# Performance work log

Hardware: AMD Instinct MI355X
Metric: run time of the kernel (lower is better)

The kernel has to match this reference:

```python
import jax, jax.numpy as jnp
import numpy as np

MARGIN = 0.2


def setup_inputs() -> dict:
    key = jax.random.key(0)
    k1, k2 = jax.random.split(key)
    B, D, C = 4096, 512, 512
    embeddings = jax.random.normal(k1, (B, D), dtype=jnp.float32)
    labels = jax.random.randint(k2, (B,), 0, C, dtype=jnp.int64)
    return {"embeddings": embeddings, "labels": labels}


def reference(embeddings, labels):
    B = embeddings.shape[0]
    # L2-normalize rows (eps matches torch F.normalize default 1e-12)
    norm = jnp.maximum(jnp.linalg.norm(embeddings, axis=1, keepdims=True), 1e-12)
    e = embeddings / norm
    # cosine distance matrix [B, B]
    dist = 1.0 - e @ e.T
    same = labels[:, None] == labels[None, :]
    eye = jnp.eye(B, dtype=bool)
    pos_mask = same & ~eye
    neg_mask = ~same
    # dist in [0, 2]; sentinels outside that range for masked reductions
    hardest_pos = jnp.max(jnp.where(pos_mask, dist, -1.0), axis=1)
    hardest_neg = jnp.min(jnp.where(neg_mask, dist, 3.0), axis=1)
    valid = jnp.any(pos_mask, axis=1) & jnp.any(neg_mask, axis=1)
    per_anchor = jax.nn.relu(hardest_pos - hardest_neg + MARGIN)
    loss_sum = jnp.sum(jnp.where(valid, per_anchor, 0.0))
    n_valid = jnp.maximum(jnp.sum(valid.astype(jnp.int32)), 1)
    return loss_sum / n_valid.astype(embeddings.dtype)
```

## Files before the change

kernel.cpp:

```cpp
#include <hip/hip_runtime.h>
#include <hip/hip_bf16.h>

#define BDIM 4096
#define DDIM 512
#define BT 128
#define BK 32
#define NKT (DDIM / BK)
#define NPAN (BDIM / BT)
#define NTRI (NPAN * (NPAN + 1) / 2)

typedef __bf16 bf16x8 __attribute__((ext_vector_type(8)));
typedef float f32x4 __attribute__((ext_vector_type(4)));
typedef unsigned short ushort_t;

__device__ inline ushort_t f2bf(float f) {
  __hip_bfloat16 h = __float2bfloat16(f);
  return *reinterpret_cast<ushort_t*>(&h);
}

__device__ inline unsigned int enc_f32(float x) {
  unsigned int u = __float_as_uint(x);
  return (u & 0x80000000u) ? ~u : (u | 0x80000000u);
}
__device__ inline float dec_f32(unsigned int e) {
  unsigned int u = (e & 0x80000000u) ? (e ^ 0x80000000u) : ~e;
  return __uint_as_float(u);
}

__global__ __launch_bounds__(256) void norm_kernel(const float* __restrict__ x,
                                                   ushort_t* __restrict__ e,
                                                   unsigned int* __restrict__ minpos_e,
                                                   unsigned int* __restrict__ maxneg_e) {
  if (blockIdx.x == 0) {
    const unsigned int init_min = enc_f32(1e30f);
    const unsigned int init_max = enc_f32(-1e30f);
    for (int i = threadIdx.x; i < BDIM; i += 256) {
      minpos_e[i] = init_min;
      maxneg_e[i] = init_max;
    }
  }
  const int row  = blockIdx.x * 4 + (threadIdx.x >> 6);
  const int lane = threadIdx.x & 63;
  const float4* xr = reinterpret_cast<const float4*>(x + (size_t)row * DDIM);
  float4 v0 = xr[lane];
  float4 v1 = xr[lane + 64];
  float ss = v0.x*v0.x + v0.y*v0.y + v0.z*v0.z + v0.w*v0.w
           + v1.x*v1.x + v1.y*v1.y + v1.z*v1.z + v1.w*v1.w;
#pragma unroll
  for (int off = 32; off >= 1; off >>= 1) ss += __shfl_xor(ss, off);
  const float inv = 1.0f / fmaxf(sqrtf(ss), 1e-12f);

  ushort4 p0, p1;
  p0.x = f2bf(v0.x * inv); p0.y = f2bf(v0.y * inv);
  p0.z = f2bf(v0.z * inv); p0.w = f2bf(v0.w * inv);
  p1.x = f2bf(v1.x * inv); p1.y = f2bf(v1.y * inv);
  p1.z = f2bf(v1.z * inv); p1.w = f2bf(v1.w * inv);
  ushort4* er = reinterpret_cast<ushort4*>(e + (size_t)row * DDIM);
  er[lane]      = p0;
  er[lane + 64] = p1;
}

#define STAGE(buf, kt)                                                         \
  do {                                                                         \
    _Pragma("unroll")                                                          \
    for (int q = 0; q < 4; ++q) {                                              \
      if (q >= 2 && diag) continue;            \
      const int off  = q * 4096 + tid * 16;                      \
      const int loff = off & 8191;                                             \
      const int row  = loff >> 6;                                              \
      const int kb   = loff & 63;                                              \
      const int pan  = (q < 2) ? Ibase : Jbase;                                \
      const char* src = (const char*)e + (size_t)(pan + row) * (DDIM * 2) +    \
                        (kt) * 64 + kb;                                        \
      __builtin_amdgcn_global_load_lds(                                        \
          (const __attribute__((address_space(1))) void*)src,                  \
          (__attribute__((address_space(3))) void*)(&Blds[buf][off]),          \
          16, 0, 0);                                                           \
    }                                                                          \
  } while (0)

__global__ __launch_bounds__(256, 4) void gemm_reduce_kernel(
    const ushort_t* __restrict__ e, const int* __restrict__ labels,
    unsigned int* __restrict__ minpos_e, unsigned int* __restrict__ maxneg_e) {
  __shared__ __align__(16) char Blds[2][16384];
  __shared__ int Llab[256];

  const int tid  = threadIdx.x;
  const int wave = tid >> 6;
  const int lane = tid & 63;
  const int l15  = lane & 15;
  const int g    = lane >> 4;
  const int wr   = wave >> 1;
  const int wc   = wave & 1;

  const int bid = blockIdx.x;
  const int t   = (bid & 7) * (NTRI / 8) + (bid >> 3);
  int I = (int)((65.0f - sqrtf(4225.0f - 8.0f * (float)t)) * 0.5f);
  while (32 * (I + 1) - ((I + 1) * I) / 2 <= t) ++I;
  while (32 * I - (I * (I - 1)) / 2 > t) --I;
  const int J = I + (t - (32 * I - (I * (I - 1)) / 2));
  const int Ibase = I * BT;
  const int Jbase = J * BT;
  const bool diag = (I == J);

  if (tid < 128) Llab[tid] = labels[Ibase + tid];
  else           Llab[tid] = labels[Jbase + tid - 128];

  f32x4 acc[4][4];
#pragma unroll
  for (int m = 0; m < 4; ++m)
#pragma unroll
    for (int n = 0; n < 4; ++n) acc[m][n] = (f32x4){0.f, 0.f, 0.f, 0.f};

  STAGE(0, 0);
  __syncthreads();

  const int bofs = diag ? 0 : 8192;
  for (int kt = 0; kt < NKT; ++kt) {
    if (kt + 1 < NKT) STAGE((kt + 1) & 1, kt + 1);

    const char* Ab = Blds[kt & 1];
    const char* Bb = Blds[kt & 1] + bofs;
    bf16x8 a[4], b[4];
#pragma unroll
    for (int m = 0; m < 4; ++m)
      a[m] = *reinterpret_cast<const bf16x8*>(
          Ab + (wr * 64 + m * 16 + l15) * 64 + g * 16);
#pragma unroll
    for (int n = 0; n < 4; ++n)
      b[n] = *reinterpret_cast<const bf16x8*>(
          Bb + (wc * 64 + n * 16 + l15) * 64 + g * 16);
#pragma unroll
    for (int m = 0; m < 4; ++m)
#pragma unroll
      for (int n = 0; n < 4; ++n)
        acc[m][n] = __builtin_amdgcn_mfma_f32_16x16x32_bf16(a[m], b[n],
                                                            acc[m][n], 0, 0, 0);
    __syncthreads();
  }

  float cmp[4], cmx[4];
  int lj[4], gj[4];
#pragma unroll
  for (int n = 0; n < 4; ++n) {
    cmp[n] = 1e30f; cmx[n] = -1e30f;
    gj[n]  = Jbase + wc * 64 + n * 16 + l15;
    lj[n]  = Llab[128 + wc * 64 + n * 16 + l15];
  }
  float rmp[4][4], rmx[4][4];
#pragma unroll
  for (int m = 0; m < 4; ++m)
#pragma unroll
    for (int r = 0; r < 4; ++r) { rmp[m][r] = 1e30f; rmx[m][r] = -1e30f; }

#pragma unroll
  for (int m = 0; m < 4; ++m) {
#pragma unroll
    for (int r = 0; r < 4; ++r) {
      const int rloc = wr * 64 + m * 16 + g * 4 + r;
      const int li   = Llab[rloc];
      const int gi   = Ibase + rloc;
#pragma unroll
      for (int n = 0; n < 4; ++n) {
        const float v = acc[m][n][r];
        if (li == lj[n]) {
          if (gi != gj[n]) {
            rmp[m][r] = fminf(rmp[m][r], v);
            cmp[n]    = fminf(cmp[n], v);
          }
        } else {
          rmx[m][r] = fmaxf(rmx[m][r], v);
          cmx[n]    = fmaxf(cmx[n], v);
        }
      }
    }
  }

#pragma unroll
  for (int off = 16; off <= 32; off <<= 1) {
#pragma unroll
    for (int n = 0; n < 4; ++n) {
      cmp[n] = fminf(cmp[n], __shfl_xor(cmp[n], off));
      cmx[n] = fmaxf(cmx[n], __shfl_xor(cmx[n], off));
    }
  }
#pragma unroll
  for (int off = 1; off < 16; off <<= 1) {
#pragma unroll
    for (int m = 0; m < 4; ++m)
#pragma unroll
      for (int r = 0; r < 4; ++r) {
        rmp[m][r] = fminf(rmp[m][r], __shfl_xor(rmp[m][r], off));
        rmx[m][r] = fmaxf(rmx[m][r], __shfl_xor(rmx[m][r], off));
      }
  }

  if (g == 0) {
#pragma unroll
    for (int n = 0; n < 4; ++n) {
      if (cmp[n] < 1e29f)  atomicMin(&minpos_e[gj[n]], enc_f32(cmp[n]));
      if (cmx[n] > -1e29f) atomicMax(&maxneg_e[gj[n]], enc_f32(cmx[n]));
    }
  }
  if (l15 == 0) {
#pragma unroll
    for (int m = 0; m < 4; ++m)
#pragma unroll
      for (int r = 0; r < 4; ++r) {
        const int gi = Ibase + wr * 64 + m * 16 + g * 4 + r;
        if (rmp[m][r] < 1e29f)  atomicMin(&minpos_e[gi], enc_f32(rmp[m][r]));
        if (rmx[m][r] > -1e29f) atomicMax(&maxneg_e[gi], enc_f32(rmx[m][r]));
      }
  }
}

__global__ __launch_bounds__(1024) void finalize_kernel(
    const unsigned int* __restrict__ minpos_e, const unsigned int* __restrict__ maxneg_e,
    float* __restrict__ out) {
  const int tid = threadIdx.x;
  float sum = 0.f;
  int cnt = 0;
  for (int row = tid; row < BDIM; row += 1024) {
    const float mp = dec_f32(minpos_e[row]);
    const float mn = dec_f32(maxneg_e[row]);
    if (mp < 1e29f && mn > -1e29f) {
      sum += fmaxf(0.f, mn - mp + 0.2f);
      cnt += 1;
    }
  }
#pragma unroll
  for (int off = 32; off >= 1; off >>= 1) {
    sum += __shfl_xor(sum, off);
    cnt += __shfl_xor(cnt, off);
  }
  __shared__ float wsum[16];
  __shared__ int   wcnt[16];
  const int wv = tid >> 6, ln = tid & 63;
  if (ln == 0) { wsum[wv] = sum; wcnt[wv] = cnt; }
  __syncthreads();
  if (tid == 0) {
    float S = 0.f; int C = 0;
    for (int w = 0; w < 16; ++w) { S += wsum[w]; C += wcnt[w]; }
    out[0] = S / (float)(C > 0 ? C : 1);
  }
}

extern "C" void kernel_launch(void* const* d_in, const int* in_sizes, int n_in,
                              void* d_out, int out_size, void* d_ws, size_t ws_size,
                              hipStream_t stream) {
  const float* x      = (const float*)d_in[0];
  const int*   labels = (const int*)d_in[1];
  float* out = (float*)d_out;

  char* ws = (char*)d_ws;
  ushort_t* e            = (ushort_t*)ws;
  unsigned int* minpos_e = (unsigned int*)(ws + (size_t)BDIM * DDIM * 2);
  unsigned int* maxneg_e = minpos_e + BDIM;

  norm_kernel<<<BDIM / 4, 256, 0, stream>>>(x, e, minpos_e, maxneg_e);
  gemm_reduce_kernel<<<NTRI, 256, 0, stream>>>(e, labels, minpos_e, maxneg_e);
  finalize_kernel<<<1, 1024, 0, stream>>>(minpos_e, maxneg_e, out);
}
```

Before: 36.68 us.

## Use 128x64 triangle tiles, triple-buffered LDS pipeline, and fused last-block finalize

The triangular 128x128 tiling becomes 128x64 tiles over the upper triangle (1056 blocks), so diagonal blocks no longer need special handling and more blocks are available for load balancing. The K loop moves to a three-stage LDS ring with explicit vmcnt waits and raw barriers, and sets MFMA priority, to overlap global-to-LDS loads with compute. Labels are now read straight from global memory instead of being staged in LDS. The separate finalize kernel is replaced by a last-block-done atomic counter inside the GEMM kernel, which saves a launch but adds a threadfence and an atomic per block.

Result: slower. 106.3 us (+189.8%).

```diff
diff --git a/kernel.cpp b/kernel.cpp
--- a/kernel.cpp
+++ b/kernel.cpp
@@ -3,16 +3,20 @@
 
 #define BDIM 4096
 #define DDIM 512
-#define BT 128
+#define BTI 128
+#define BTJ 64
 #define BK 32
 #define NKT (DDIM / BK)
-#define NPAN (BDIM / BT)
-#define NTRI (NPAN * (NPAN + 1) / 2)
+#define NBLK 1056
 
 typedef __bf16 bf16x8 __attribute__((ext_vector_type(8)));
 typedef float f32x4 __attribute__((ext_vector_type(4)));
 typedef unsigned short ushort_t;
 
+#define WAITV3() asm volatile("s_waitcnt vmcnt(3)" ::: "memory")
+#define WAITV0() asm volatile("s_waitcnt vmcnt(0)" ::: "memory")
+#define WAITL0() asm volatile("s_waitcnt lgkmcnt(0)" ::: "memory")
+
 __device__ inline ushort_t f2bf(float f) {
   __hip_bfloat16 h = __float2bfloat16(f);
   return *reinterpret_cast<ushort_t*>(&h);
@@ -30,7 +34,8 @@
 __global__ __launch_bounds__(256) void norm_kernel(const float* __restrict__ x,
                                                    ushort_t* __restrict__ e,
                                                    unsigned int* __restrict__ minpos_e,
-                                                   unsigned int* __restrict__ maxneg_e) {
+                                                   unsigned int* __restrict__ maxneg_e,
+                                                   unsigned int* __restrict__ done_ctr) {
   if (blockIdx.x == 0) {
     const unsigned int init_min = enc_f32(1e30f);
     const unsigned int init_max = enc_f32(-1e30f);
@@ -38,6 +43,7 @@
       minpos_e[i] = init_min;
       maxneg_e[i] = init_max;
     }
+    if (threadIdx.x == 0) done_ctr[0] = 0u;
   }
   const int row  = blockIdx.x * 4 + (threadIdx.x >> 6);
   const int lane = threadIdx.x & 63;
@@ -60,30 +66,39 @@
   er[lane + 64] = p1;
 }
 
-#define STAGE(buf, kt)                                                         \
+#define STAGE(bi, kt)                                                          \
   do {                                                                         \
     _Pragma("unroll")                                                          \
-    for (int q = 0; q < 4; ++q) {                                              \
-      if (q >= 2 && diag) continue;            \
-      const int off  = q * 4096 + tid * 16;                      \
-      const int loff = off & 8191;                                             \
-      const int row  = loff >> 6;                                              \
-      const int kb   = loff & 63;                                              \
-      const int pan  = (q < 2) ? Ibase : Jbase;                                \
-      const char* src = (const char*)e + (size_t)(pan + row) * (DDIM * 2) +    \
-                        (kt) * 64 + kb;                                        \
+    for (int q = 0; q < 2; ++q) {                          \
+      const int off = q * 4096 + tid * 16;                                     \
+      const int row = off >> 6;                                                \
+      const char* src = (const char*)e + (size_t)(Ibase + row) * (DDIM * 2) +  \
+                        (kt) * 64 + (off & 63);                                \
       __builtin_amdgcn_global_load_lds(                                        \
           (const __attribute__((address_space(1))) void*)src,                  \
-          (__attribute__((address_space(3))) void*)(&Blds[buf][off]),          \
+          (__attribute__((address_space(3))) void*)(&Blds[bi][off]),           \
+          16, 0, 0);                                                           \
+    }                                                                          \
+    {                                                       \
+      const int boff = tid * 16;                                               \
+      const int brow = boff >> 6;                                              \
+      const char* bsrc = (const char*)e + (size_t)(Jbase + brow) * (DDIM * 2) +\
+                         (kt) * 64 + (boff & 63);                              \
+      __builtin_amdgcn_global_load_lds(                                        \
+          (const __attribute__((address_space(1))) void*)bsrc,                 \
+          (__attribute__((address_space(3))) void*)(&Blds[bi][8192 + boff]),   \
           16, 0, 0);                                                           \
     }                                                                          \
   } while (0)
 
 __global__ __launch_bounds__(256, 4) void gemm_reduce_kernel(
     const ushort_t* __restrict__ e, const int* __restrict__ labels,
-    unsigned int* __restrict__ minpos_e, unsigned int* __restrict__ maxneg_e) {
-  __shared__ __align__(16) char Blds[2][16384];
-  __shared__ int Llab[256];
+    unsigned int* __restrict__ minpos_e, unsigned int* __restrict__ maxneg_e,
+    unsigned int* __restrict__ done_ctr, float* __restrict__ out) {
+  __shared__ __align__(16) char Blds[3][12288];
+  __shared__ int lastflag;
+  __shared__ float wsum[4];
+  __shared__ int   wcnt[4];
 
   const int tid  = threadIdx.x;
   const int wave = tid >> 6;
@@ -94,58 +109,61 @@
   const int wc   = wave & 1;
 
   const int bid = blockIdx.x;
-  const int t   = (bid & 7) * (NTRI / 8) + (bid >> 3);
-  int I = (int)((65.0f - sqrtf(4225.0f - 8.0f * (float)t)) * 0.5f);
-  while (32 * (I + 1) - ((I + 1) * I) / 2 <= t) ++I;
-  while (32 * I - (I * (I - 1)) / 2 > t) --I;
-  const int J = I + (t - (32 * I - (I * (I - 1)) / 2));
-  const int Ibase = I * BT;
-  const int Jbase = J * BT;
-  const bool diag = (I == J);
-
-  if (tid < 128) Llab[tid] = labels[Ibase + tid];
-  else           Llab[tid] = labels[Jbase + tid - 128];
-
-  f32x4 acc[4][4];
+  const int t   = (bid & 7) * (NBLK / 8) + (bid >> 3);
+  int I = (int)((65.0f - sqrtf(4225.0f - 4.0f * (float)t)) * 0.5f);
+  if (I < 0) I = 0;
+  if (I > 31) I = 31;
+  while (I < 31 && (I + 1) * (65 - (I + 1)) <= t) ++I;
+  while (I > 0 && I * (65 - I) > t) --I;
+  const int h = 2 * I + (t - I * (65 - I));
+  const int Ibase = I * BTI;
+  const int Jbase = h * BTJ;
+
+  f32x4 acc[4][2];
 #pragma unroll
   for (int m = 0; m < 4; ++m)
 #pragma unroll
-    for (int n = 0; n < 4; ++n) acc[m][n] = (f32x4){0.f, 0.f, 0.f, 0.f};
+    for (int n = 0; n < 2; ++n) acc[m][n] = (f32x4){0.f, 0.f, 0.f, 0.f};
 
   STAGE(0, 0);
-  __syncthreads();
-
-  const int bofs = diag ? 0 : 8192;
+  STAGE(1, 1);
+
+#pragma unroll
   for (int kt = 0; kt < NKT; ++kt) {
-    if (kt + 1 < NKT) STAGE((kt + 1) & 1, kt + 1);
-
-    const char* Ab = Blds[kt & 1];
-    const char* Bb = Blds[kt & 1] + bofs;
-    bf16x8 a[4], b[4];
-#pragma unroll
-    for (int m = 0; m < 4; ++m)
-      a[m] = *reinterpret_cast<const bf16x8*>(
-          Ab + (wr * 64 + m * 16 + l15) * 64 + g * 16);
-#pragma unroll
-    for (int n = 0; n < 4; ++n)
-      b[n] = *reinterpret_cast<const bf16x8*>(
-          Bb + (wc * 64 + n * 16 + l15) * 64 + g * 16);
-#pragma unroll
-    for (int m = 0; m < 4; ++m)
-#pragma unroll
-      for (int n = 0; n < 4; ++n)
+    if (kt < NKT - 1) { WAITV3(); } else { WAITV0(); }
+    WAITL0();
+    __builtin_amdgcn_sched_barrier(0);
+    __builtin_amdgcn_s_barrier();
+    __builtin_amdgcn_sched_barrier(0);
+    if (kt + 2 < NKT) STAGE((kt + 2) % 3, kt + 2);
+
+    const char* Ab = Blds[kt % 3];
+    const char* Bb = Ab + 8192;
+    bf16x8 a[4], b[2];
+#pragma unroll
+    for (int m = 0; m < 4; ++m)
+      a[m] = *reinterpret_cast<const bf16x8*>(Ab + (wr * 64 + m * 16 + l15) * 64 + g * 16);
+#pragma unroll
+    for (int n = 0; n < 2; ++n)
+      b[n] = *reinterpret_cast<const bf16x8*>(Bb + (wc * 32 + n * 16 + l15) * 64 + g * 16);
+
+    __builtin_amdgcn_s_setprio(1);
+#pragma unroll
+    for (int m = 0; m < 4; ++m)
+#pragma unroll
+      for (int n = 0; n < 2; ++n)
         acc[m][n] = __builtin_amdgcn_mfma_f32_16x16x32_bf16(a[m], b[n],
                                                             acc[m][n], 0, 0, 0);
-    __syncthreads();
-  }
-
-  float cmp[4], cmx[4];
-  int lj[4], gj[4];
-#pragma unroll
-  for (int n = 0; n < 4; ++n) {
+    __builtin_amdgcn_s_setprio(0);
+  }
+
+  float cmp[2], cmx[2];
+  int lj[2], gj[2];
+#pragma unroll
+  for (int n = 0; n < 2; ++n) {
     cmp[n] = 1e30f; cmx[n] = -1e30f;
-    gj[n]  = Jbase + wc * 64 + n * 16 + l15;
-    lj[n]  = Llab[128 + wc * 64 + n * 16 + l15];
+    gj[n]  = Jbase + wc * 32 + n * 16 + l15;
+    lj[n]  = labels[gj[n]];
   }
   float rmp[4][4], rmx[4][4];
 #pragma unroll
@@ -157,11 +175,10 @@
   for (int m = 0; m < 4; ++m) {
 #pragma unroll
     for (int r = 0; r < 4; ++r) {
-      const int rloc = wr * 64 + m * 16 + g * 4 + r;
-      const int li   = Llab[rloc];
-      const int gi   = Ibase + rloc;
-#pragma unroll
-      for (int n = 0; n < 4; ++n) {
+      const int gi = Ibase + wr * 64 + m * 16 + g * 4 + r;
+      const int li = labels[gi];
+#pragma unroll
+      for (int n = 0; n < 2; ++n) {
         const float v = acc[m][n][r];
         if (li == lj[n]) {
           if (gi != gj[n]) {
@@ -179,7 +196,7 @@
 #pragma unroll
   for (int off = 16; off <= 32; off <<= 1) {
 #pragma unroll
-    for (int n = 0; n < 4; ++n) {
+    for (int n = 0; n < 2; ++n) {
       cmp[n] = fminf(cmp[n], __shfl_xor(cmp[n], off));
       cmx[n] = fmaxf(cmx[n], __shfl_xor(cmx[n], off));
     }
@@ -197,7 +214,7 @@
 
   if (g == 0) {
 #pragma unroll
-    for (int n = 0; n < 4; ++n) {
+    for (int n = 0; n < 2; ++n) {
       if (cmp[n] < 1e29f)  atomicMin(&minpos_e[gj[n]], enc_f32(cmp[n]));
       if (cmx[n] > -1e29f) atomicMax(&maxneg_e[gj[n]], enc_f32(cmx[n]));
     }
@@ -212,36 +229,38 @@
         if (rmx[m][r] > -1e29f) atomicMax(&maxneg_e[gi], enc_f32(rmx[m][r]));
       }
   }
-}
-
-__global__ __launch_bounds__(1024) void finalize_kernel(
-    const unsigned int* __restrict__ minpos_e, const unsigned int* __restrict__ maxneg_e,
-    float* __restrict__ out) {
-  const int tid = threadIdx.x;
-  float sum = 0.f;
-  int cnt = 0;
-  for (int row = tid; row < BDIM; row += 1024) {
-    const float mp = dec_f32(minpos_e[row]);
-    const float mn = dec_f32(maxneg_e[row]);
-    if (mp < 1e29f && mn > -1e29f) {
-      sum += fmaxf(0.f, mn - mp + 0.2f);
-      cnt += 1;
-    }
-  }
-#pragma unroll
-  for (int off = 32; off >= 1; off >>= 1) {
-    sum += __shfl_xor(sum, off);
-    cnt += __shfl_xor(cnt, off);
-  }
-  __shared__ float wsum[16];
-  __shared__ int   wcnt[16];
-  const int wv = tid >> 6, ln = tid & 63;
-  if (ln == 0) { wsum[wv] = sum; wcnt[wv] = cnt; }
+
+  __threadfence();
+  if (tid == 0) lastflag = (atomicAdd(done_ctr, 1u) == NBLK - 1);
   __syncthreads();
-  if (tid == 0) {
-    float S = 0.f; int C = 0;
-    for (int w = 0; w < 16; ++w) { S += wsum[w]; C += wcnt[w]; }
-    out[0] = S / (float)(C > 0 ? C : 1);
+  if (lastflag) {
+    __threadfence();
+    float sum = 0.f;
+    int cnt = 0;
+    for (int row = tid; row < BDIM; row += 256) {
+      const unsigned int ump = __hip_atomic_load(&minpos_e[row], __ATOMIC_RELAXED,
+                                                 __HIP_MEMORY_SCOPE_AGENT);
+      const unsigned int umn = __hip_atomic_load(&maxneg_e[row], __ATOMIC_RELAXED,
+                                                 __HIP_MEMORY_SCOPE_AGENT);
+      const float mp = dec_f32(ump);
+      const float mn = dec_f32(umn);
+      if (mp < 1e29f && mn > -1e29f) {
+        sum += fmaxf(0.f, mn - mp + 0.2f);
+        cnt += 1;
+      }
+    }
+#pragma unroll
+    for (int off = 32; off >= 1; off >>= 1) {
+      sum += __shfl_xor(sum, off);
+      cnt += __shfl_xor(cnt, off);
+    }
+    if (lane == 0) { wsum[wave] = sum; wcnt[wave] = cnt; }
+    __syncthreads();
+    if (tid == 0) {
+      float S = 0.f; int C = 0;
+      for (int w = 0; w < 4; ++w) { S += wsum[w]; C += wcnt[w]; }
+      out[0] = S / (float)(C > 0 ? C : 1);
+    }
   }
 }
 
@@ -256,8 +275,9 @@
   ushort_t* e            = (ushort_t*)ws;
   unsigned int* minpos_e = (unsigned int*)(ws + (size_t)BDIM * DDIM * 2);
   unsigned int* maxneg_e = minpos_e + BDIM;
-
-  norm_kernel<<<BDIM / 4, 256, 0, stream>>>(x, e, minpos_e, maxneg_e);
-  gemm_reduce_kernel<<<NTRI, 256, 0, stream>>>(e, labels, minpos_e, maxneg_e);
-  finalize_kernel<<<1, 1024, 0, stream>>>(minpos_e, maxneg_e, out);
-}
+  unsigned int* done_ctr = maxneg_e + BDIM;
+
+  norm_kernel<<<BDIM / 4, 256, 0, stream>>>(x, e, minpos_e, maxneg_e, done_ctr);
+  gemm_reduce_kernel<<<NBLK, 256, 0, stream>>>(e, labels, minpos_e, maxneg_e,
+                                               done_ctr, out);
+}
```
